# Optimization experiments

Measured on AMD Instinct MI355X. Metric: run time of the kernel, lower is better.

The kernel has to match this reference:

```python
import jax, jax.numpy as jnp
import numpy as np

N = 50000
E = 500000
NIN, NHID, NOUT = 256, 128, 64


def setup_inputs() -> dict:
    key = jax.random.key(0)
    ks = jax.random.split(key, 6)
    x = jax.random.normal(ks[0], (N, NIN), dtype=jnp.float32)
    edge_index = jax.random.randint(ks[1], (2, E), 0, N, dtype=jnp.int64)
    # GCNConv weights (glorot-ish scale) and biases
    W1 = jax.random.normal(ks[2], (NIN, NHID), dtype=jnp.float32) / np.sqrt(NIN)
    b1 = jnp.zeros((NHID,), dtype=jnp.float32)
    W2 = jax.random.normal(ks[3], (NHID, NHID), dtype=jnp.float32) / np.sqrt(NHID)
    b2 = jnp.zeros((NHID,), dtype=jnp.float32)
    # decoder Linear
    Wd = jax.random.normal(ks[4], (NHID, NOUT), dtype=jnp.float32) / np.sqrt(NHID)
    bd = jnp.zeros((NOUT,), dtype=jnp.float32)
    return {"x": x, "edge_index": edge_index, "W1": W1, "b1": b1,
            "W2": W2, "b2": b2, "Wd": Wd, "bd": bd}


def _gcn_norm(edge_index, n):
    # add self-loops, then symmetric normalization deg^-1/2 * deg^-1/2
    loops = jnp.arange(n, dtype=edge_index.dtype)
    src = jnp.concatenate([edge_index[0], loops])
    dst = jnp.concatenate([edge_index[1], loops])
    deg = jax.ops.segment_sum(jnp.ones_like(dst, dtype=jnp.float32), dst,
                              num_segments=n)
    dis = jnp.where(deg > 0, jax.lax.rsqrt(deg), 0.0)
    norm = dis[src] * dis[dst]  # [E + N]
    return src, dst, norm


def _gcn_conv(h, W, b, src, dst, norm, n):
    h = h @ W                              # [N, out]
    msg = h[src] * norm[:, None]           # gather + scale  [E+N, out]
    agg = jax.ops.segment_sum(msg, dst, num_segments=n)  # scatter-add
    return agg + b


def reference(x, edge_index, W1, b1, W2, b2, Wd, bd):
    n = x.shape[0]
    src, dst, norm = _gcn_norm(edge_index, n)
    h = jax.nn.relu(_gcn_conv(x, W1, b1, src, dst, norm, n))
    h = jax.nn.relu(_gcn_conv(h, W2, b2, src, dst, norm, n))
    # dropout is a no-op in eval mode
    out = h @ Wd + bd
    return out, h
```

## Files before the change

kernel.cpp:

```cpp
#include <hip/hip_runtime.h>

#define NIN 256
#define NHID 128
#define NOUT 64
#define CAP 64

typedef __attribute__((ext_vector_type(8))) short bf16x8;
typedef __attribute__((ext_vector_type(4))) float f32x4;

__device__ __forceinline__ unsigned int bf16_rne(float v) {
    unsigned int b = __float_as_uint(v);
    return (b + 0x7fffu + ((b >> 16) & 1u)) >> 16;
}
__device__ __forceinline__ float bf16_to_f(unsigned int bits16) {
    return __uint_as_float(bits16 << 16);
}

__device__ __forceinline__ void pack_dev(const float* __restrict__ W,
                                         uint4* __restrict__ hi, uint4* __restrict__ lo,
                                         int K, int N, int idx) {
    int lane = idx & 63;
    int f = idx >> 6;
    int nct = N / 16;
    int ct = f % nct;
    int kt = f / nct;
    int col = ct * 16 + (lane & 15);
    int k0 = kt * 32 + (lane >> 4) * 8;
    unsigned int hs[8], ls[8];
#pragma unroll
    for (int e = 0; e < 8; ++e) {
        float v = W[(size_t)(k0 + e) * N + col];
        unsigned int h = bf16_rne(v);
        float hf = __uint_as_float(h << 16);
        ls[e] = bf16_rne(v - hf);
        hs[e] = h;
    }
    uint4 hv, lv;
    hv.x = hs[0] | (hs[1] << 16); hv.y = hs[2] | (hs[3] << 16);
    hv.z = hs[4] | (hs[5] << 16); hv.w = hs[6] | (hs[7] << 16);
    lv.x = ls[0] | (ls[1] << 16); lv.y = ls[2] | (ls[3] << 16);
    lv.z = ls[4] | (ls[5] << 16); lv.w = ls[6] | (ls[7] << 16);
    hi[idx] = hv;
    lo[idx] = lv;
}

__global__ __launch_bounds__(256) void setup_kernel(int* __restrict__ cursor,
                                                    const float* __restrict__ W1,
                                                    const float* __restrict__ W2,
                                                    const float* __restrict__ Wd,
                                                    uint4* __restrict__ w1hi, uint4* __restrict__ w1lo,
                                                    uint4* __restrict__ w2hi, uint4* __restrict__ w2lo,
                                                    uint4* __restrict__ wdhi, uint4* __restrict__ wdlo,
                                                    int n, int GZ) {
    int bid = blockIdx.x;
    int t = threadIdx.x;
    if (bid < GZ) {
        int i = bid * 256 + t;
        if (i < n) cursor[i] = 0;
    } else {
        int pidx = (bid - GZ) * 256 + t;
        if (pidx < 4096)       pack_dev(W1, w1hi, w1lo, NIN,  NHID, pidx);
        else if (pidx < 6144)  pack_dev(W2, w2hi, w2lo, NHID, NHID, pidx - 4096);
        else                   pack_dev(Wd, wdhi, wdlo, NHID, NOUT, pidx - 6144);
    }
}

__global__ __launch_bounds__(256) void mega_kernel(const float* __restrict__ x,
                                                   const int* __restrict__ src,
                                                   const int* __restrict__ dst,
                                                   int* __restrict__ cursor,
                                                   int* __restrict__ bucket,
                                                   const uint4* __restrict__ Bhi,
                                                   const uint4* __restrict__ Blo,
                                                   unsigned int* __restrict__ bufA,
                                                   int n, int E, int GG) {
    constexpr int NKT = NIN / 32;
    constexpr int NCT = NHID / 16;
    __shared__ uint4 lds_b[2][NCT][64];

    int bid = blockIdx.x;
    int t = threadIdx.x;

    if (bid >= GG) {
        int e = (bid - GG) * 256 + t;
        if (e < E) {
            int d = dst[e];
            int pos = atomicAdd(&cursor[d], 1);
            if (pos < CAP) bucket[(size_t)d * CAP + pos] = src[e];
        }
        return;
    }

    int lane = t & 63;
    int w = t >> 6;
    int row0 = bid * 64 + w * 16;
    bool rowok = row0 < n;
    int arow = row0 + (lane & 15);
    int kbase = (lane >> 4) * 8;

    f32x4 acc[NCT];
#pragma unroll
    for (int c = 0; c < NCT; ++c)
#pragma unroll
        for (int r = 0; r < 4; ++r) acc[c][r] = 0.f;

    for (int kt = 0; kt < NKT; ++kt) {
        __syncthreads();
        {
            const uint4* sh = Bhi + (size_t)kt * NCT * 64;
            const uint4* sl = Blo + (size_t)kt * NCT * 64;
            uint4* dh = &lds_b[0][0][0];
            uint4* dl = &lds_b[1][0][0];
            for (int i = t; i < NCT * 64; i += 256) {
                dh[i] = sh[i];
                dl[i] = sl[i];
            }
        }
        __syncthreads();

        bf16x8 ahi, alo;
        {
            float va[8];
            if (rowok) {
                const float* xp = x + (size_t)arow * NIN + kt * 32 + kbase;
                float4 v0 = *(const float4*)xp;
                float4 v1 = *(const float4*)(xp + 4);
                va[0] = v0.x; va[1] = v0.y; va[2] = v0.z; va[3] = v0.w;
                va[4] = v1.x; va[5] = v1.y; va[6] = v1.z; va[7] = v1.w;
            } else {
#pragma unroll
                for (int e = 0; e < 8; ++e) va[e] = 0.f;
            }
#pragma unroll
            for (int e = 0; e < 8; ++e) {
                unsigned int h = bf16_rne(va[e]);
                float hf = __uint_as_float(h << 16);
                unsigned int l = bf16_rne(va[e] - hf);
                ahi[e] = (short)h;
                alo[e] = (short)l;
            }
        }

#pragma unroll
        for (int c = 0; c < NCT; ++c) {
            bf16x8 bhi = *(const bf16x8*)&lds_b[0][c][lane];
            bf16x8 blo = *(const bf16x8*)&lds_b[1][c][lane];
            acc[c] = __builtin_amdgcn_mfma_f32_16x16x32_bf16(ahi, bhi, acc[c], 0, 0, 0);
            acc[c] = __builtin_amdgcn_mfma_f32_16x16x32_bf16(ahi, blo, acc[c], 0, 0, 0);
            acc[c] = __builtin_amdgcn_mfma_f32_16x16x32_bf16(alo, bhi, acc[c], 0, 0, 0);
        }
    }

    if (rowok) {
        int rbase = row0 + (lane >> 4) * 4;
        int cbase = lane & 15;
        unsigned short* Y = (unsigned short*)bufA;
#pragma unroll
        for (int c = 0; c < NCT; ++c) {
            int col = c * 16 + cbase;
#pragma unroll
            for (int r = 0; r < 4; ++r)
                Y[(size_t)(rbase + r) * NHID + col] = (unsigned short)bf16_rne(acc[c][r]);
        }
    }
}

template<int K, int NCOL, bool BIAS, bool XBF, bool OBF>
__global__ __launch_bounds__(256) void gemm_mfma_kernel(const void* __restrict__ Xv,
                                                        const uint4* __restrict__ Bhi,
                                                        const uint4* __restrict__ Blo,
                                                        const float* __restrict__ bias,
                                                        void* __restrict__ Yv, int nrows) {
    constexpr int NKT = K / 32;
    constexpr int NCT = NCOL / 16;
    __shared__ uint4 lds_b[2][NCT][64];

    int t = threadIdx.x;
    int lane = t & 63;
    int w = t >> 6;
    int row0 = blockIdx.x * 64 + w * 16;
    bool rowok = row0 < nrows;
    int arow = row0 + (lane & 15);
    int kbase = (lane >> 4) * 8;

    f32x4 acc[NCT];
#pragma unroll
    for (int c = 0; c < NCT; ++c)
#pragma unroll
        for (int r = 0; r < 4; ++r) acc[c][r] = 0.f;

    for (int kt = 0; kt < NKT; ++kt) {
        __syncthreads();
        {
            const uint4* sh = Bhi + (size_t)kt * NCT * 64;
            const uint4* sl = Blo + (size_t)kt * NCT * 64;
            uint4* dh = &lds_b[0][0][0];
            uint4* dl = &lds_b[1][0][0];
            for (int i = t; i < NCT * 64; i += 256) {
                dh[i] = sh[i];
                dl[i] = sl[i];
            }
        }
        __syncthreads();

        bf16x8 ahi, alo;
        if constexpr (XBF) {
            const unsigned short* X = (const unsigned short*)Xv;
            if (rowok)
                ahi = *(const bf16x8*)(X + (size_t)arow * K + kt * 32 + kbase);
            else
#pragma unroll
                for (int e = 0; e < 8; ++e) ahi[e] = 0;
        } else {
            const float* X = (const float*)Xv;
            float va[8];
            if (rowok) {
                const float* xp = X + (size_t)arow * K + kt * 32 + kbase;
                float4 v0 = *(const float4*)xp;
                float4 v1 = *(const float4*)(xp + 4);
                va[0] = v0.x; va[1] = v0.y; va[2] = v0.z; va[3] = v0.w;
                va[4] = v1.x; va[5] = v1.y; va[6] = v1.z; va[7] = v1.w;
            } else {
#pragma unroll
                for (int e = 0; e < 8; ++e) va[e] = 0.f;
            }
#pragma unroll
            for (int e = 0; e < 8; ++e) {
                unsigned int h = bf16_rne(va[e]);
                float hf = __uint_as_float(h << 16);
                unsigned int l = bf16_rne(va[e] - hf);
                ahi[e] = (short)h;
                alo[e] = (short)l;
            }
        }

#pragma unroll
        for (int c = 0; c < NCT; ++c) {
            bf16x8 bhi = *(const bf16x8*)&lds_b[0][c][lane];
            bf16x8 blo = *(const bf16x8*)&lds_b[1][c][lane];
            acc[c] = __builtin_amdgcn_mfma_f32_16x16x32_bf16(ahi, bhi, acc[c], 0, 0, 0);
            acc[c] = __builtin_amdgcn_mfma_f32_16x16x32_bf16(ahi, blo, acc[c], 0, 0, 0);
            if constexpr (!XBF)
                acc[c] = __builtin_amdgcn_mfma_f32_16x16x32_bf16(alo, bhi, acc[c], 0, 0, 0);
        }
    }

    if (rowok) {
        int rbase = row0 + (lane >> 4) * 4;
        int cbase = lane & 15;
#pragma unroll
        for (int c = 0; c < NCT; ++c) {
            int col = c * 16 + cbase;
            float bv = BIAS ? bias[col] : 0.f;
#pragma unroll
            for (int r = 0; r < 4; ++r) {
                float v = acc[c][r] + bv;
                if constexpr (OBF)
                    ((unsigned short*)Yv)[(size_t)(rbase + r) * NCOL + col] =
                        (unsigned short)bf16_rne(v);
                else
                    ((float*)Yv)[(size_t)(rbase + r) * NCOL + col] = v;
            }
        }
    }
}

__global__ __launch_bounds__(256) void agg_kernel(const unsigned int* __restrict__ Hb,
                                                  const int* __restrict__ cursor,
                                                  const int* __restrict__ bucket,
                                                  const float* __restrict__ bias,
                                                  unsigned int* __restrict__ Yb,
                                                  float* __restrict__ Yf, int n) {
    int node = (blockIdx.x * 256 + threadIdx.x) >> 6;
    int lane = threadIdx.x & 63;
    if (node >= n) return;

    int deg = cursor[node];
    float di = rsqrtf((float)(deg + 1));
    unsigned int su = Hb[(size_t)node * 64 + lane];
    int c = min(deg, CAP);

    int s = 0;
    float wl = 0.f;
    if (lane < c) {
        s = bucket[(size_t)node * CAP + lane];
        wl = rsqrtf((float)(cursor[s] + 1));
    }

    float ax[8], ay[8];
#pragma unroll
    for (int u = 0; u < 8; ++u) { ax[u] = 0.f; ay[u] = 0.f; }
    ax[0] = bf16_to_f(su & 0xffffu) * di;
    ay[0] = bf16_to_f(su >> 16) * di;

    for (int jj = 0; jj < c; jj += 8) {
        int   sv[8];
        float wv[8];
#pragma unroll
        for (int u = 0; u < 8; ++u) {
            sv[u] = __shfl(s, jj + u, 64);
            wv[u] = __shfl(wl, jj + u, 64);
        }
        unsigned int vv[8];
#pragma unroll
        for (int u = 0; u < 8; ++u)
            vv[u] = Hb[(size_t)sv[u] * 64 + lane];
#pragma unroll
        for (int u = 0; u < 8; ++u) {
            ax[u] += bf16_to_f(vv[u] & 0xffffu) * wv[u];
            ay[u] += bf16_to_f(vv[u] >> 16) * wv[u];
        }
    }

    float2 b = ((const float2*)bias)[lane];
    float rx = (((ax[0] + ax[1]) + (ax[2] + ax[3])) + ((ax[4] + ax[5]) + (ax[6] + ax[7]))) * di + b.x;
    float ry = (((ay[0] + ay[1]) + (ay[2] + ay[3])) + ((ay[4] + ay[5]) + (ay[6] + ay[7]))) * di + b.y;
    rx = fmaxf(rx, 0.f);
    ry = fmaxf(ry, 0.f);
    Yb[(size_t)node * 64 + lane] = bf16_rne(rx) | (bf16_rne(ry) << 16);
    if (Yf) {
        float2 o; o.x = rx; o.y = ry;
        ((float2*)(Yf + (size_t)node * NHID))[lane] = o;
    }
}


extern "C" void kernel_launch(void* const* d_in, const int* in_sizes, int n_in,
                              void* d_out, int out_size, void* d_ws, size_t ws_size,
                              hipStream_t stream) {
    const float* x  = (const float*)d_in[0];
    const int*   ei = (const int*)d_in[1];
    const float* W1 = (const float*)d_in[2];
    const float* b1 = (const float*)d_in[3];
    const float* W2 = (const float*)d_in[4];
    const float* b2 = (const float*)d_in[5];
    const float* Wd = (const float*)d_in[6];
    const float* bd = (const float*)d_in[7];

    int n = in_sizes[0] / NIN;
    int E = in_sizes[1] / 2;
    const int* src = ei;
    const int* dst = ei + E;

    char* ws = (char*)d_ws;
    size_t off = 0;
    auto alloc = [&](size_t bytes) -> void* {
        void* p = ws + off;
        off += (bytes + 255) & ~(size_t)255;
        return p;
    };
    int*   cursor = (int*)alloc((size_t)n * 4);
    int*   bucket = (int*)alloc((size_t)n * CAP * 4);
    unsigned int* bufA = (unsigned int*)alloc((size_t)n * 64 * 4);
    unsigned int* h1b  = (unsigned int*)alloc((size_t)n * 64 * 4);
    unsigned int* bufB = (unsigned int*)alloc((size_t)n * 64 * 4);
    unsigned int* h2b  = (unsigned int*)alloc((size_t)n * 64 * 4);
    uint4* w1hi = (uint4*)alloc((size_t)(NIN / 32) * (NHID / 16) * 64 * 16);
    uint4* w1lo = (uint4*)alloc((size_t)(NIN / 32) * (NHID / 16) * 64 * 16);
    uint4* w2hi = (uint4*)alloc((size_t)(NHID / 32) * (NHID / 16) * 64 * 16);
    uint4* w2lo = (uint4*)alloc((size_t)(NHID / 32) * (NHID / 16) * 64 * 16);
    uint4* wdhi = (uint4*)alloc((size_t)(NHID / 32) * (NOUT / 16) * 64 * 16);
    uint4* wdlo = (uint4*)alloc((size_t)(NHID / 32) * (NOUT / 16) * 64 * 16);

    float* out  = (float*)d_out;
    float* hout = out + (size_t)n * NOUT;

    int GZ = (n + 255) / 256;
    int GG = (n + 63) / 64;
    int GF = (E + 255) / 256;
    int gGemm = GG;
    int gAgg = (n + 3) / 4;

    setup_kernel<<<GZ + 28, 256, 0, stream>>>(cursor, W1, W2, Wd,
                                              w1hi, w1lo, w2hi, w2lo, wdhi, wdlo, n, GZ);

    mega_kernel<<<GG + GF, 256, 0, stream>>>(x, src, dst, cursor, bucket,
                                             w1hi, w1lo, bufA, n, E, GG);

    agg_kernel<<<gAgg, 256, 0, stream>>>(bufA, cursor, bucket, b1, h1b, nullptr, n);

    gemm_mfma_kernel<NHID, NHID, false, true, true><<<gGemm, 256, 0, stream>>>(
        h1b, w2hi, w2lo, nullptr, bufB, n);
    agg_kernel<<<gAgg, 256, 0, stream>>>(bufB, cursor, bucket, b2, h2b, hout, n);

    gemm_mfma_kernel<NHID, NOUT, true, true, false><<<gGemm, 256, 0, stream>>>(
        h2b, wdhi, wdlo, bd, out, n);
}
```

Measured before the change: 118.7 us.

## Build per-range LDS-atomic edge buckets and precompute per-node degree norms

Replaces the global-atomic bucket fill (one atomicAdd per edge on a global cursor array, plus a separate zeroing pass) with 128 blocks that each own a node range and an edge chunk and do their atomics in shared memory. Each node gets 8 sub-buckets of 16 slots, and per-chunk counts are stored as bytes. The degree rsqrt is now computed once per node into a dis array inside the first GEMM launch, so agg reads it instead of recomputing rsqrt from the neighbour's cursor. The cost is that every build block scans its whole edge chunk (16x redundant reads of dst), agg has to compact the sub-buckets per lane, and the fixed NPRMAX shared array assumes n/16 <= 3136.

```diff
diff --git a/kernel.cpp b/kernel.cpp
--- a/kernel.cpp
+++ b/kernel.cpp
@@ -3,7 +3,10 @@
 #define NIN 256
 #define NHID 128
 #define NOUT 64
-#define CAP 64
+#define RNG 16
+#define CHK 8
+#define CAP8 16
+#define NPRMAX 3136
 
 typedef __attribute__((ext_vector_type(8))) short bf16x8;
 typedef __attribute__((ext_vector_type(4))) float f32x4;
@@ -14,6 +17,9 @@
 }
 __device__ __forceinline__ float bf16_to_f(unsigned int bits16) {
     return __uint_as_float(bits16 << 16);
+}
+__device__ __forceinline__ int sum4b(unsigned int u) {
+    return (u & 255) + ((u >> 8) & 255) + ((u >> 16) & 255) + ((u >> 24) & 255);
 }
 
 __device__ __forceinline__ void pack_dev(const float* __restrict__ W,
@@ -44,36 +50,58 @@
     lo[idx] = lv;
 }
 
-__global__ __launch_bounds__(256) void setup_kernel(int* __restrict__ cursor,
-                                                    const float* __restrict__ W1,
-                                                    const float* __restrict__ W2,
-                                                    const float* __restrict__ Wd,
-                                                    uint4* __restrict__ w1hi, uint4* __restrict__ w1lo,
-                                                    uint4* __restrict__ w2hi, uint4* __restrict__ w2lo,
-                                                    uint4* __restrict__ wdhi, uint4* __restrict__ wdlo,
-                                                    int n, int GZ) {
+__global__ __launch_bounds__(256) void buildpack_kernel(
+        const int* __restrict__ src, const int* __restrict__ dst,
+        int* __restrict__ bucket, unsigned char* __restrict__ cnt8,
+        const float* __restrict__ W1, const float* __restrict__ W2,
+        const float* __restrict__ Wd,
+        uint4* __restrict__ w1hi, uint4* __restrict__ w1lo,
+        uint4* __restrict__ w2hi, uint4* __restrict__ w2lo,
+        uint4* __restrict__ wdhi, uint4* __restrict__ wdlo,
+        int n, int E) {
+    __shared__ int cur[NPRMAX];
     int bid = blockIdx.x;
     int t = threadIdx.x;
-    if (bid < GZ) {
-        int i = bid * 256 + t;
-        if (i < n) cursor[i] = 0;
+
+    if (bid < RNG * CHK) {
+        int r = bid / CHK;
+        int c = bid % CHK;
+        int npr_rt = (n + RNG - 1) / RNG;
+        int base = r * npr_rt;
+        int npr = min(npr_rt, n - base);
+        if (npr <= 0) return;
+        for (int i = t; i < npr; i += 256) cur[i] = 0;
+        __syncthreads();
+
+        int ec0 = (int)(((long long)c * E) / CHK);
+        int ec1 = (int)(((long long)(c + 1) * E) / CHK);
+        for (int i = ec0 + t; i < ec1; i += 256) {
+            int d = dst[i];
+            unsigned int rel = (unsigned int)(d - base);
+            if (rel < (unsigned int)npr) {
+                int pos = atomicAdd(&cur[rel], 1);
+                if (pos < CAP8)
+                    bucket[((size_t)d * CHK + c) * CAP8 + pos] = src[i];
+            }
+        }
+        __syncthreads();
+        for (int i = t; i < npr; i += 256)
+            cnt8[(size_t)(base + i) * CHK + c] = (unsigned char)min(cur[i], 255);
     } else {
-        int pidx = (bid - GZ) * 256 + t;
+        int pidx = (bid - RNG * CHK) * 256 + t;
         if (pidx < 4096)       pack_dev(W1, w1hi, w1lo, NIN,  NHID, pidx);
         else if (pidx < 6144)  pack_dev(W2, w2hi, w2lo, NHID, NHID, pidx - 4096);
         else                   pack_dev(Wd, wdhi, wdlo, NHID, NOUT, pidx - 6144);
     }
 }
 
-__global__ __launch_bounds__(256) void mega_kernel(const float* __restrict__ x,
-                                                   const int* __restrict__ src,
-                                                   const int* __restrict__ dst,
-                                                   int* __restrict__ cursor,
-                                                   int* __restrict__ bucket,
-                                                   const uint4* __restrict__ Bhi,
-                                                   const uint4* __restrict__ Blo,
-                                                   unsigned int* __restrict__ bufA,
-                                                   int n, int E, int GG) {
+__global__ __launch_bounds__(256) void mega1_kernel(const float* __restrict__ x,
+                                                    const uint4* __restrict__ Bhi,
+                                                    const uint4* __restrict__ Blo,
+                                                    unsigned int* __restrict__ bufA,
+                                                    const unsigned char* __restrict__ cnt8,
+                                                    float* __restrict__ dis,
+                                                    int n, int GG) {
     constexpr int NKT = NIN / 32;
     constexpr int NCT = NHID / 16;
     __shared__ uint4 lds_b[2][NCT][64];
@@ -82,11 +110,11 @@
     int t = threadIdx.x;
 
     if (bid >= GG) {
-        int e = (bid - GG) * 256 + t;
-        if (e < E) {
-            int d = dst[e];
-            int pos = atomicAdd(&cursor[d], 1);
-            if (pos < CAP) bucket[(size_t)d * CAP + pos] = src[e];
+        int i = (bid - GG) * 256 + t;
+        if (i < n) {
+            uint2 cb = *(const uint2*)(cnt8 + (size_t)i * CHK);
+            int deg = sum4b(cb.x) + sum4b(cb.y);
+            dis[i] = rsqrtf((float)(deg + 1));
         }
         return;
     }
@@ -266,8 +294,9 @@
 }
 
 __global__ __launch_bounds__(256) void agg_kernel(const unsigned int* __restrict__ Hb,
-                                                  const int* __restrict__ cursor,
+                                                  const unsigned char* __restrict__ cnt8,
                                                   const int* __restrict__ bucket,
+                                                  const float* __restrict__ dis,
                                                   const float* __restrict__ bias,
                                                   unsigned int* __restrict__ Yb,
                                                   float* __restrict__ Yf, int n) {
@@ -275,16 +304,25 @@
     int lane = threadIdx.x & 63;
     if (node >= n) return;
 
-    int deg = cursor[node];
-    float di = rsqrtf((float)(deg + 1));
+    float di = dis[node];
     unsigned int su = Hb[(size_t)node * 64 + lane];
-    int c = min(deg, CAP);
+
+    uint2 cb = *(const uint2*)(cnt8 + (size_t)node * CHK);
+    int ksel = -1, jsel = 0, P = 0;
+#pragma unroll
+    for (int k = 0; k < CHK; ++k) {
+        int ck = (int)((k < 4 ? (cb.x >> (8 * k)) : (cb.y >> (8 * (k - 4)))) & 255u);
+        ck = min(ck, CAP8);
+        if (lane >= P && lane < P + ck) { ksel = k; jsel = lane - P; }
+        P += ck;
+    }
+    int cnt = P;
 
     int s = 0;
     float wl = 0.f;
-    if (lane < c) {
-        s = bucket[(size_t)node * CAP + lane];
-        wl = rsqrtf((float)(cursor[s] + 1));
+    if (ksel >= 0) {
+        s = bucket[((size_t)node * CHK + ksel) * CAP8 + jsel];
+        wl = dis[s];
     }
 
     float ax[8], ay[8];
@@ -293,7 +331,7 @@
     ax[0] = bf16_to_f(su & 0xffffu) * di;
     ay[0] = bf16_to_f(su >> 16) * di;
 
-    for (int jj = 0; jj < c; jj += 8) {
+    for (int jj = 0; jj < cnt; jj += 8) {
         int   sv[8];
         float wv[8];
 #pragma unroll
@@ -349,8 +387,9 @@
         off += (bytes + 255) & ~(size_t)255;
         return p;
     };
-    int*   cursor = (int*)alloc((size_t)n * 4);
-    int*   bucket = (int*)alloc((size_t)n * CAP * 4);
+    int* bucket          = (int*)alloc((size_t)n * CHK * CAP8 * 4);
+    unsigned char* cnt8  = (unsigned char*)alloc((size_t)n * CHK);
+    float* dis           = (float*)alloc((size_t)n * 4);
     unsigned int* bufA = (unsigned int*)alloc((size_t)n * 64 * 4);
     unsigned int* h1b  = (unsigned int*)alloc((size_t)n * 64 * 4);
     unsigned int* bufB = (unsigned int*)alloc((size_t)n * 64 * 4);
@@ -365,24 +404,22 @@
     float* out  = (float*)d_out;
     float* hout = out + (size_t)n * NOUT;
 
-    int GZ = (n + 255) / 256;
     int GG = (n + 63) / 64;
-    int GF = (E + 255) / 256;
-    int gGemm = GG;
+    int GD = (n + 255) / 256;
     int gAgg = (n + 3) / 4;
 
-    setup_kernel<<<GZ + 28, 256, 0, stream>>>(cursor, W1, W2, Wd,
-                                              w1hi, w1lo, w2hi, w2lo, wdhi, wdlo, n, GZ);
-
-    mega_kernel<<<GG + GF, 256, 0, stream>>>(x, src, dst, cursor, bucket,
-                                             w1hi, w1lo, bufA, n, E, GG);
-
-    agg_kernel<<<gAgg, 256, 0, stream>>>(bufA, cursor, bucket, b1, h1b, nullptr, n);
-
-    gemm_mfma_kernel<NHID, NHID, false, true, true><<<gGemm, 256, 0, stream>>>(
+    buildpack_kernel<<<RNG * CHK + 28, 256, 0, stream>>>(
+        src, dst, bucket, cnt8, W1, W2, Wd,
+        w1hi, w1lo, w2hi, w2lo, wdhi, wdlo, n, E);
+
+    mega1_kernel<<<GG + GD, 256, 0, stream>>>(x, w1hi, w1lo, bufA, cnt8, dis, n, GG);
+
+    agg_kernel<<<gAgg, 256, 0, stream>>>(bufA, cnt8, bucket, dis, b1, h1b, nullptr, n);
+
+    gemm_mfma_kernel<NHID, NHID, false, true, true><<<GG, 256, 0, stream>>>(
         h1b, w2hi, w2lo, nullptr, bufB, n);
-    agg_kernel<<<gAgg, 256, 0, stream>>>(bufB, cursor, bucket, b2, h2b, hout, n);
-
-    gemm_mfma_kernel<NHID, NOUT, true, true, false><<<gGemm, 256, 0, stream>>>(
+    agg_kernel<<<gAgg, 256, 0, stream>>>(bufB, cnt8, bucket, dis, b2, h2b, hout, n);
+
+    gemm_mfma_kernel<NHID, NOUT, true, true, false><<<GG, 256, 0, stream>>>(
         h2b, wdhi, wdlo, bd, out, n);
 }
```

New measurement: 223.2 us. 88.1% more time.
